# Optimization experiments

Measured on AMD Instinct MI355X. Metric: run time of the kernel, lower is better.

## Reference

```python
import jax, jax.numpy as jnp
import numpy as np

B, N, D, D_OUT = 4, 512, 48, 48

def setup_inputs() -> dict:
    key = jax.random.key(0)
    ks = jax.random.split(key, 7)
    s1 = 1.0 / np.sqrt(2 * D)
    s2 = 1.0 / np.sqrt(2 * D)
    s3 = 1.0 / np.sqrt(D)
    return {
        "x": jax.random.normal(ks[0], (B, N, D), dtype=jnp.float32),
        "W1": jax.random.uniform(ks[1], (2 * D, 2 * D), jnp.float32, -s1, s1),
        "b1": jax.random.uniform(ks[2], (2 * D,), jnp.float32, -s1, s1),
        "W2": jax.random.uniform(ks[3], (2 * D, D), jnp.float32, -s2, s2),
        "b2": jax.random.uniform(ks[4], (D,), jnp.float32, -s2, s2),
        "W3": jax.random.uniform(ks[5], (D, D_OUT), jnp.float32, -s3, s3),
        "b3": jax.random.uniform(ks[6], (D_OUT,), jnp.float32, -s3, s3),
    }

def reference(x, W1, b1, W2, b2, W3, b3):
    # x: [B, N, D]
    Bn, Nn, Dn = x.shape
    xi = jnp.broadcast_to(x[:, :, None, :], (Bn, Nn, Nn, Dn))  # row i
    xj = jnp.broadcast_to(x[:, None, :, :], (Bn, Nn, Nn, Dn))  # col j
    pair = jnp.concatenate([xi, xj], axis=-1)  # [B,N,N,2D]
    h = jax.nn.gelu(pair @ W1 + b1, approximate=False)
    h = jax.nn.gelu(h @ W2 + b2, approximate=False)
    pair_out = h @ W3 + b3  # [B,N,N,d_out]
    mask = jnp.triu(jnp.ones((Nn, Nn), dtype=bool), 1)  # j > i masked
    pair_out = jnp.where(mask[None, :, :, None], 0.0, pair_out)
    w = jnp.linalg.norm(pair_out, axis=-1)  # [B,N,N]
    w = jnp.where(mask[None, :, :], -1e9, w)
    w = jax.nn.softmax(w, axis=-1)
    return jnp.einsum('bnj,bnjd->bnd', w, pair_out)
```

## Files before the change

### kernel.cpp

```cpp
#include <hip/hip_runtime.h>
#include <hip/hip_bf16.h>


constexpr int BATCH = 4;
constexpr int SEQ   = 512;
constexpr int DIM   = 48;
constexpr int DIM2  = 96;
constexpr int CH    = 64;

constexpr int AW  = 104;
constexpr int HW  = 72;

typedef short short8v __attribute__((ext_vector_type(8)));
typedef float float4v __attribute__((ext_vector_type(4)));
typedef unsigned int uint2v __attribute__((ext_vector_type(2)));

#define MFMA16(a, b, c) __builtin_amdgcn_mfma_f32_16x16x32_bf16(a, b, c, 0, 0, 0)

__device__ __forceinline__ float gelu_tanh(float x) {
    float u = x * x;
    float q = fmaf(0.10294537f, u, 2.3022077f);
    float e = __builtin_amdgcn_exp2f(x * q);
    float r = __builtin_amdgcn_rcpf(e + 1.0f);
    return fmaf(-x, r, x);
}
__device__ __forceinline__ short f2bf1(float v) {
    return (short)((__float_as_uint(v) + 0x8000u) >> 16);
}
__device__ __forceinline__ unsigned pack_bf16x2(float a, float b) {
    unsigned ua = __float_as_uint(a) + 0x8000u;
    unsigned ub = __float_as_uint(b) + 0x8000u;
    return __builtin_amdgcn_perm(ub, ua, 0x07060302u);
}
constexpr float LOG2E = 1.4426950408889634f;

__global__ __launch_bounds__(192) void uv_kernel(
    const float* __restrict__ x, const float* __restrict__ W1,
    const float* __restrict__ b1, float* __restrict__ U, float* __restrict__ V)
{
    __shared__ float sxT[DIM * 4];
    const int t = threadIdx.x;
    const int row0 = blockIdx.x * 4;
    if (t < DIM * 4) {
        int r = t / DIM, m = t - r * DIM;
        sxT[m * 4 + r] = x[(row0 + r) * DIM + m];
    }
    __syncthreads();
    const bool isU = (t < DIM2);
    const int  k   = isU ? t : (t - DIM2);
    const float* Wcol = W1 + (isU ? 0 : DIM * DIM2) + k;
    float binit = isU ? b1[k] : 0.0f;
    float a0 = binit, a1 = binit, a2 = binit, a3 = binit;
    #pragma unroll 8
    for (int m = 0; m < DIM; ++m) {
        float wv = Wcol[m * DIM2];
        const float4 xa = *(const float4*)&sxT[m * 4];
        a0 = fmaf(wv, xa.x, a0); a1 = fmaf(wv, xa.y, a1);
        a2 = fmaf(wv, xa.z, a2); a3 = fmaf(wv, xa.w, a3);
    }
    float* dst = isU ? U : V;
    dst[(row0 + 0) * DIM2 + k] = a0; dst[(row0 + 1) * DIM2 + k] = a1;
    dst[(row0 + 2) * DIM2 + k] = a2; dst[(row0 + 3) * DIM2 + k] = a3;
}

__global__ __launch_bounds__(256, 4) void pair_kernel(
    const float* __restrict__ U, const float* __restrict__ V,
    const float* __restrict__ W2, const float* __restrict__ b2,
    const float* __restrict__ W3, const float* __restrict__ b3,
    float* __restrict__ out)
{
    __shared__ __align__(16) char smem[23296];
    short* sA  = (short*)smem;
    short* sH  = (short*)(smem + 13312);
    float* sUi = (float*)(smem + 22528);

    const int t   = threadIdx.x;
    const int bid = blockIdx.x;
    const int b   = bid & (BATCH - 1);
    const int i   = (SEQ - 1) - (bid >> 2);
    const int rowbase = b * SEQ + i;

    const int lane = t & 63;
    const int w    = t >> 6;
    const int col  = lane & 15;
    const int quad = lane >> 4;
    const int qo   = quad * 8;
    const int m4   = w * 16 + col;
    const int rbase = w * 16 + quad * 4;

    for (int idx = t; idx < DIM2 * DIM; idx += 256) {
        int k = idx / DIM, n = idx - k * DIM;
        sA[n * AW + k] = f2bf1(W2[idx]);
    }
    for (int idx = t; idx < DIM * DIM; idx += 256) {
        int k = idx / DIM, n = idx - k * DIM;
        sH[n * HW + k] = f2bf1(W3[idx]);
    }
    for (int idx = t; idx < CH * 16; idx += 256)
        sH[(idx >> 4) * HW + 48 + (idx & 15)] = 0;
    if (t < DIM2) sUi[t] = U[rowbase * DIM2 + t];
    __syncthreads();

    const short* w2b = sA + col * AW + qo;
    const short8v w200 = *(const short8v*)(w2b + 0);
    const short8v w201 = *(const short8v*)(w2b + 32);
    const short8v w202 = *(const short8v*)(w2b + 64);
    const short8v w210 = *(const short8v*)(w2b + 16*AW + 0);
    const short8v w211 = *(const short8v*)(w2b + 16*AW + 32);
    const short8v w212 = *(const short8v*)(w2b + 16*AW + 64);
    const short8v w220 = *(const short8v*)(w2b + 32*AW + 0);
    const short8v w221 = *(const short8v*)(w2b + 32*AW + 32);
    const short8v w222 = *(const short8v*)(w2b + 32*AW + 64);
    const short* w3b = sH + col * HW + qo;
    const short8v w300 = *(const short8v*)(w3b + 0);
    const short8v w301 = *(const short8v*)(w3b + 32);
    const short8v w310 = *(const short8v*)(w3b + 16*HW + 0);
    const short8v w311 = *(const short8v*)(w3b + 16*HW + 32);
    const short8v w320 = *(const short8v*)(w3b + 32*HW + 0);
    const short8v w321 = *(const short8v*)(w3b + 32*HW + 32);
    const float bb20 = b2[col], bb21 = b2[16 + col], bb22 = b2[32 + col];
    const float bb30 = b3[col], bb31 = b3[16 + col], bb32 = b3[32 + col];
    __syncthreads();

    const int pr = t >> 2;
    const int pq = t & 3;

    float acc0 = 0.f, acc1 = 0.f, acc2 = 0.f;
    float m_run = -1e30f, l_run = 0.0f;

    for (int j0 = 0; j0 + (w << 4) <= i; j0 += CH) {
        const int jmax = i - j0;

        {
            const float* Vb = V + (b * SEQ + j0 + pr) * DIM2 + pq * 4;
            #pragma unroll
            for (int kk = 0; kk < 6; ++kk) {
                const float4 vv = *(const float4*)(Vb + 16 * kk);
                const float4 uu = *(const float4*)&sUi[(pq + 4 * kk) * 4];
                float g0 = gelu_tanh(uu.x + vv.x);
                float g1 = gelu_tanh(uu.y + vv.y);
                float g2 = gelu_tanh(uu.z + vv.z);
                float g3 = gelu_tanh(uu.w + vv.w);
                uint2v o;
                o.x = pack_bf16x2(g0, g1);
                o.y = pack_bf16x2(g2, g3);
                *(uint2v*)&sA[pr * AW + (pq + 4 * kk) * 4] = o;
            }
        }

        {
            const short* arow = &sA[m4 * AW + qo];
            short8v a0 = *(const short8v*)(arow + 0);
            short8v a1 = *(const short8v*)(arow + 32);
            short8v a2 = *(const short8v*)(arow + 64);
            float4v c0 = {0.f,0.f,0.f,0.f}, c1 = c0, c2 = c0;
            c0 = MFMA16(a0, w200, c0); c0 = MFMA16(a1, w201, c0); c0 = MFMA16(a2, w202, c0);
            c1 = MFMA16(a0, w210, c1); c1 = MFMA16(a1, w211, c1); c1 = MFMA16(a2, w212, c1);
            c2 = MFMA16(a0, w220, c2); c2 = MFMA16(a1, w221, c2); c2 = MFMA16(a2, w222, c2);
            #pragma unroll
            for (int r = 0; r < 4; ++r) {
                sH[(rbase + r) * HW +  0 + col] = f2bf1(gelu_tanh(c0[r] + bb20));
                sH[(rbase + r) * HW + 16 + col] = f2bf1(gelu_tanh(c1[r] + bb21));
                sH[(rbase + r) * HW + 32 + col] = f2bf1(gelu_tanh(c2[r] + bb22));
            }
        }

        {
            const short* hrw = &sH[m4 * HW + qo];
            short8v a0 = *(const short8v*)(hrw + 0);
            short8v a1 = *(const short8v*)(hrw + 32);
            float4v c0 = {0.f,0.f,0.f,0.f}, c1 = c0, c2 = c0;
            c0 = MFMA16(a0, w300, c0); c0 = MFMA16(a1, w301, c0);
            c1 = MFMA16(a0, w310, c1); c1 = MFMA16(a1, w311, c1);
            c2 = MFMA16(a0, w320, c2); c2 = MFMA16(a1, w321, c2);
            float4v p0, p1, p2;
            float vr[4];
            #pragma unroll
            for (int r = 0; r < 4; ++r) {
                p0[r] = c0[r] + bb30; p1[r] = c1[r] + bb31; p2[r] = c2[r] + bb32;
                float ss = p0[r]*p0[r] + p1[r]*p1[r] + p2[r]*p2[r];
                ss += __shfl_xor(ss, 1);
                ss += __shfl_xor(ss, 2);
                ss += __shfl_xor(ss, 4);
                ss += __shfl_xor(ss, 8);
                vr[r] = (rbase + r <= jmax) ? __builtin_amdgcn_sqrtf(ss) : -1e30f;
            }
            float mloc = fmaxf(fmaxf(vr[0], vr[1]), fmaxf(vr[2], vr[3]));
            mloc = fmaxf(mloc, __shfl_xor(mloc, 16));
            mloc = fmaxf(mloc, __shfl_xor(mloc, 32));
            float newm = fmaxf(m_run, mloc);
            float sc = __builtin_amdgcn_exp2f((m_run - newm) * LOG2E);
            float e0 = __builtin_amdgcn_exp2f((vr[0] - newm) * LOG2E);
            float e1 = __builtin_amdgcn_exp2f((vr[1] - newm) * LOG2E);
            float e2 = __builtin_amdgcn_exp2f((vr[2] - newm) * LOG2E);
            float e3 = __builtin_amdgcn_exp2f((vr[3] - newm) * LOG2E);
            float s = (e0 + e1) + (e2 + e3);
            s += __shfl_xor(s, 16);
            s += __shfl_xor(s, 32);
            l_run = fmaf(l_run, sc, s);
            m_run = newm;
            acc0 *= sc; acc1 *= sc; acc2 *= sc;
            acc0 = fmaf(e0, p0[0], acc0); acc1 = fmaf(e0, p1[0], acc1); acc2 = fmaf(e0, p2[0], acc2);
            acc0 = fmaf(e1, p0[1], acc0); acc1 = fmaf(e1, p1[1], acc1); acc2 = fmaf(e1, p2[1], acc2);
            acc0 = fmaf(e2, p0[2], acc0); acc1 = fmaf(e2, p1[2], acc1); acc2 = fmaf(e2, p2[2], acc2);
            acc0 = fmaf(e3, p0[3], acc0); acc1 = fmaf(e3, p1[3], acc1); acc2 = fmaf(e3, p2[3], acc2);
        }
    }

    acc0 += __shfl_xor(acc0, 16); acc0 += __shfl_xor(acc0, 32);
    acc1 += __shfl_xor(acc1, 16); acc1 += __shfl_xor(acc1, 32);
    acc2 += __shfl_xor(acc2, 16); acc2 += __shfl_xor(acc2, 32);
    float* red = (float*)smem;
    __syncthreads();
    if (lane < 16) {
        red[w * 64 + lane]      = acc0;
        red[w * 64 + 16 + lane] = acc1;
        red[w * 64 + 32 + lane] = acc2;
    }
    if (lane == 0) { red[w * 64 + 48] = m_run; red[w * 64 + 49] = l_run; }
    __syncthreads();
    if (t < DIM) {
        float mm0 = red[48],       mm1 = red[64 + 48];
        float mm2 = red[128 + 48], mm3 = red[192 + 48];
        float M = fmaxf(fmaxf(mm0, mm1), fmaxf(mm2, mm3));
        float f0 = __builtin_amdgcn_exp2f((mm0 - M) * LOG2E);
        float f1 = __builtin_amdgcn_exp2f((mm1 - M) * LOG2E);
        float f2 = __builtin_amdgcn_exp2f((mm2 - M) * LOG2E);
        float f3 = __builtin_amdgcn_exp2f((mm3 - M) * LOG2E);
        float num = f0 * red[t] + f1 * red[64 + t] + f2 * red[128 + t] + f3 * red[192 + t];
        float den = f0 * red[49] + f1 * red[64 + 49] + f2 * red[128 + 49] + f3 * red[192 + 49];
        out[rowbase * DIM + t] = num / den;
    }
}

extern "C" void kernel_launch(void* const* d_in, const int* in_sizes, int n_in,
                              void* d_out, int out_size, void* d_ws, size_t ws_size,
                              hipStream_t stream) {
    const float* x  = (const float*)d_in[0];
    const float* W1 = (const float*)d_in[1];
    const float* b1 = (const float*)d_in[2];
    const float* W2 = (const float*)d_in[3];
    const float* b2 = (const float*)d_in[4];
    const float* W3 = (const float*)d_in[5];
    const float* b3 = (const float*)d_in[6];
    float* out = (float*)d_out;

    float* U = (float*)d_ws;
    float* V = U + BATCH * SEQ * DIM2;

    uv_kernel<<<BATCH * SEQ / 4, 192, 0, stream>>>(x, W1, b1, U, V);
    pair_kernel<<<BATCH * SEQ, 256, 0, stream>>>(U, V, W2, b2, W3, b3, out);
}
```

Measured before the change: 107.5 us.

## Replace GELU with LDS lookup table and reload third W2 fragment per tile

Replaces the exp/rcp tanh-approximate GELU with a 256-entry linearly interpolated table of exact GELU stored in LDS, clamped to [-8, 8]. The third K-slice of W2 goes into a separate LDS buffer and is reloaded every chunk instead of living in registers. This cuts VGPR pressure at the cost of extra LDS reads. The U+V gelu stage now writes 16-byte vectors. The table trades transcendental ALU work for LDS gathers that may bank-conflict, and its piecewise-linear accuracy differs from the previous approximation.

After: 115.3 us. +7.2%, slower.

```diff
diff --git a/kernel.cpp b/kernel.cpp
--- a/kernel.cpp
+++ b/kernel.cpp
@@ -10,19 +10,31 @@
 
 constexpr int AW  = 104;
 constexpr int HW  = 72;
+constexpr int W2H_LD = 40;
+
+constexpr int OFF_SA   = 0;
+constexpr int OFF_SH   = 13312;
+constexpr int OFF_SUI  = 22528;
+constexpr int OFF_W2H  = 22912;
+constexpr int OFF_TAB  = 26752;
+constexpr int LDS_SIZE = 28800;
 
 typedef short short8v __attribute__((ext_vector_type(8)));
 typedef float float4v __attribute__((ext_vector_type(4)));
-typedef unsigned int uint2v __attribute__((ext_vector_type(2)));
+typedef unsigned int uint4vv __attribute__((ext_vector_type(4)));
 
 #define MFMA16(a, b, c) __builtin_amdgcn_mfma_f32_16x16x32_bf16(a, b, c, 0, 0, 0)
 
-__device__ __forceinline__ float gelu_tanh(float x) {
-    float u = x * x;
-    float q = fmaf(0.10294537f, u, 2.3022077f);
-    float e = __builtin_amdgcn_exp2f(x * q);
-    float r = __builtin_amdgcn_rcpf(e + 1.0f);
-    return fmaf(-x, r, x);
+__device__ __forceinline__ float gelu_exact(float x) {
+    return 0.5f * x * (1.0f + erff(x * 0.70710678118654752440f));
+}
+__device__ __forceinline__ float gelu_tbl(float x, const float2* tab) {
+    float m = fmaf(x, 16.0f, 128.0f);
+    m = fminf(fmaxf(m, 0.0f), 255.999f);
+    int   idx = (int)m;
+    float f   = m - (float)idx;
+    float2 e  = tab[idx];
+    return fmaf(f, e.y, e.x);
 }
 __device__ __forceinline__ short f2bf1(float v) {
     return (short)((__float_as_uint(v) + 0x8000u) >> 16);
@@ -69,10 +81,12 @@
     const float* __restrict__ W3, const float* __restrict__ b3,
     float* __restrict__ out)
 {
-    __shared__ __align__(16) char smem[23296];
-    short* sA  = (short*)smem;
-    short* sH  = (short*)(smem + 13312);
-    float* sUi = (float*)(smem + 22528);
+    __shared__ __align__(16) char smem[LDS_SIZE];
+    short* sA   = (short*)(smem + OFF_SA);
+    short* sH   = (short*)(smem + OFF_SH);
+    float* sUi  = (float*)(smem + OFF_SUI);
+    short* W2HI = (short*)(smem + OFF_W2H);
+    const float2* TAB = (const float2*)(smem + OFF_TAB);
 
     const int t   = threadIdx.x;
     const int bid = blockIdx.x;
@@ -98,19 +112,29 @@
     }
     for (int idx = t; idx < CH * 16; idx += 256)
         sH[(idx >> 4) * HW + 48 + (idx & 15)] = 0;
+    for (int idx = t; idx < 32 * DIM; idx += 256) {
+        int kk = idx / DIM;
+        int n  = idx - kk * DIM;
+        W2HI[n * W2H_LD + kk] = f2bf1(W2[(64 + kk) * DIM + n]);
+    }
+    {
+        float x0 = (float)(t & 255) * 0.0625f - 8.0f;
+        if (t < 256) {
+            float g0 = gelu_exact(x0);
+            float g1 = gelu_exact(x0 + 0.0625f);
+            ((float2*)(smem + OFF_TAB))[t] = make_float2(g0, g1 - g0);
+        }
+    }
     if (t < DIM2) sUi[t] = U[rowbase * DIM2 + t];
     __syncthreads();
 
     const short* w2b = sA + col * AW + qo;
     const short8v w200 = *(const short8v*)(w2b + 0);
     const short8v w201 = *(const short8v*)(w2b + 32);
-    const short8v w202 = *(const short8v*)(w2b + 64);
     const short8v w210 = *(const short8v*)(w2b + 16*AW + 0);
     const short8v w211 = *(const short8v*)(w2b + 16*AW + 32);
-    const short8v w212 = *(const short8v*)(w2b + 16*AW + 64);
     const short8v w220 = *(const short8v*)(w2b + 32*AW + 0);
     const short8v w221 = *(const short8v*)(w2b + 32*AW + 32);
-    const short8v w222 = *(const short8v*)(w2b + 32*AW + 64);
     const short* w3b = sH + col * HW + qo;
     const short8v w300 = *(const short8v*)(w3b + 0);
     const short8v w301 = *(const short8v*)(w3b + 32);
@@ -120,6 +144,7 @@
     const short8v w321 = *(const short8v*)(w3b + 32*HW + 32);
     const float bb20 = b2[col], bb21 = b2[16 + col], bb22 = b2[32 + col];
     const float bb30 = b3[col], bb31 = b3[16 + col], bb32 = b3[32 + col];
+    const short* w2h = W2HI + col * W2H_LD + qo;
     __syncthreads();
 
     const int pr = t >> 2;
@@ -132,36 +157,48 @@
         const int jmax = i - j0;
 
         {
-            const float* Vb = V + (b * SEQ + j0 + pr) * DIM2 + pq * 4;
+            const float* Vb = V + (b * SEQ + j0 + pr) * DIM2 + pq * 24;
+            const float* Ub = sUi + pq * 24;
             #pragma unroll
-            for (int kk = 0; kk < 6; ++kk) {
-                const float4 vv = *(const float4*)(Vb + 16 * kk);
-                const float4 uu = *(const float4*)&sUi[(pq + 4 * kk) * 4];
-                float g0 = gelu_tanh(uu.x + vv.x);
-                float g1 = gelu_tanh(uu.y + vv.y);
-                float g2 = gelu_tanh(uu.z + vv.z);
-                float g3 = gelu_tanh(uu.w + vv.w);
-                uint2v o;
+            for (int jj = 0; jj < 3; ++jj) {
+                const float4 v0 = *(const float4*)(Vb + jj * 8);
+                const float4 v1 = *(const float4*)(Vb + jj * 8 + 4);
+                const float4 u0 = *(const float4*)(Ub + jj * 8);
+                const float4 u1 = *(const float4*)(Ub + jj * 8 + 4);
+                float g0 = gelu_tbl(u0.x + v0.x, TAB);
+                float g1 = gelu_tbl(u0.y + v0.y, TAB);
+                float g2 = gelu_tbl(u0.z + v0.z, TAB);
+                float g3 = gelu_tbl(u0.w + v0.w, TAB);
+                float g4 = gelu_tbl(u1.x + v1.x, TAB);
+                float g5 = gelu_tbl(u1.y + v1.y, TAB);
+                float g6 = gelu_tbl(u1.z + v1.z, TAB);
+                float g7 = gelu_tbl(u1.w + v1.w, TAB);
+                uint4vv o;
                 o.x = pack_bf16x2(g0, g1);
                 o.y = pack_bf16x2(g2, g3);
-                *(uint2v*)&sA[pr * AW + (pq + 4 * kk) * 4] = o;
+                o.z = pack_bf16x2(g4, g5);
+                o.w = pack_bf16x2(g6, g7);
+                *(uint4vv*)&sA[pr * AW + pq * 24 + jj * 8] = o;
             }
         }
 
         {
+            const short8v f202 = *(const short8v*)(w2h + 0);
+            const short8v f212 = *(const short8v*)(w2h + 16 * W2H_LD);
+            const short8v f222 = *(const short8v*)(w2h + 32 * W2H_LD);
             const short* arow = &sA[m4 * AW + qo];
             short8v a0 = *(const short8v*)(arow + 0);
             short8v a1 = *(const short8v*)(arow + 32);
             short8v a2 = *(const short8v*)(arow + 64);
             float4v c0 = {0.f,0.f,0.f,0.f}, c1 = c0, c2 = c0;
-            c0 = MFMA16(a0, w200, c0); c0 = MFMA16(a1, w201, c0); c0 = MFMA16(a2, w202, c0);
-            c1 = MFMA16(a0, w210, c1); c1 = MFMA16(a1, w211, c1); c1 = MFMA16(a2, w212, c1);
-            c2 = MFMA16(a0, w220, c2); c2 = MFMA16(a1, w221, c2); c2 = MFMA16(a2, w222, c2);
+            c0 = MFMA16(a0, w200, c0); c0 = MFMA16(a1, w201, c0); c0 = MFMA16(a2, f202, c0);
+            c1 = MFMA16(a0, w210, c1); c1 = MFMA16(a1, w211, c1); c1 = MFMA16(a2, f212, c1);
+            c2 = MFMA16(a0, w220, c2); c2 = MFMA16(a1, w221, c2); c2 = MFMA16(a2, f222, c2);
             #pragma unroll
             for (int r = 0; r < 4; ++r) {
-                sH[(rbase + r) * HW +  0 + col] = f2bf1(gelu_tanh(c0[r] + bb20));
-                sH[(rbase + r) * HW + 16 + col] = f2bf1(gelu_tanh(c1[r] + bb21));
-                sH[(rbase + r) * HW + 32 + col] = f2bf1(gelu_tanh(c2[r] + bb22));
+                sH[(rbase + r) * HW +  0 + col] = f2bf1(gelu_tbl(c0[r] + bb20, TAB));
+                sH[(rbase + r) * HW + 16 + col] = f2bf1(gelu_tbl(c1[r] + bb21, TAB));
+                sH[(rbase + r) * HW + 32 + col] = f2bf1(gelu_tbl(c2[r] + bb22, TAB));
             }
         }
 
```
